# Kernel optimization log

Hardware: AMD Instinct MI355X
Metric: run time of the kernel (lower is better)

## Reference

```python
import jax, jax.numpy as jnp
import numpy as np

B, FH, FW, T = 128, 26, 26, 50
A, NUM_CLASSES = 5, 20
IGNORE_THRESH = 0.75
COORD_SCALE, NOOBJ_SCALE, OBJ_SCALE, CLASS_SCALE = 1.0, 1.0, 5.0, 1.0
ANCHORS = jnp.array([[1.3221, 1.73145], [3.19275, 4.00944], [5.05587, 8.09892],
                     [9.47112, 4.84053], [11.2364, 10.0071]], dtype=jnp.float32)


def xywh2xxyy(b):
    return jnp.stack([b[:, 0] - b[:, 2] / 2, b[:, 1] - b[:, 3] / 2,
                      b[:, 0] + b[:, 2] / 2, b[:, 1] + b[:, 3] / 2], axis=1)


def xxyy2xywh(b):
    return jnp.stack([(b[:, 0] + b[:, 2]) / 2, (b[:, 1] + b[:, 3]) / 2,
                      b[:, 2] - b[:, 0], b[:, 3] - b[:, 1]], axis=1)


def pair_iou(b1, b2):
    # b1: [N,4] xxyy, b2: [K,4] xxyy -> [N,K]
    xi1 = jnp.maximum(b1[:, None, 0], b2[None, :, 0])
    yi1 = jnp.maximum(b1[:, None, 1], b2[None, :, 1])
    xi2 = jnp.minimum(b1[:, None, 2], b2[None, :, 2])
    yi2 = jnp.minimum(b1[:, None, 3], b2[None, :, 3])
    inter = jnp.maximum(xi2 - xi1, 0.0) * jnp.maximum(yi2 - yi1, 0.0)
    a1 = ((b1[:, 2] - b1[:, 0]) * (b1[:, 3] - b1[:, 1]))[:, None]
    a2 = ((b2[:, 2] - b2[:, 0]) * (b2[:, 3] - b2[:, 1]))[None, :]
    return inter / (a1 + a2 - inter)


def make_all_anchors(F_H, F_W):
    ys, xs = jnp.meshgrid(jnp.arange(F_H), jnp.arange(F_W), indexing='ij')
    cells = jnp.stack([xs.ravel(), ys.ravel()], axis=-1).astype(jnp.float32)  # [K,2] (c_x, c_y)
    K = F_H * F_W
    all_anch = jnp.concatenate([jnp.broadcast_to(cells[:, None, :], (K, A, 2)),
                                jnp.broadcast_to(ANCHORS[None, :, :], (K, A, 2))], axis=-1)
    return all_anch.reshape(K * A, 4)  # (c_x, c_y, p_w, p_h), top-left-cell coords


def _build_target_single(box_deltas, gt, all_anch, anch_xxyy, F_H, F_W):
    # box_deltas: [K*A,4] (sig tx, sig ty, exp tw, exp th); gt: [T,5]
    K = F_H * F_W
    valid = gt[:, :4].sum(-1) > 0
    scale = jnp.array([F_W, F_H, F_W, F_H], dtype=jnp.float32)
    gt_xxyy = gt[:, :4] * scale  # [T,4] grid units
    # predicted boxes
    pred = jnp.stack([all_anch[:, 0] + box_deltas[:, 0], all_anch[:, 1] + box_deltas[:, 1],
                      all_anch[:, 2] * box_deltas[:, 2], all_anch[:, 3] * box_deltas[:, 3]], axis=1)
    pred_xxyy = xywh2xxyy(pred)
    ious = pair_iou(pred_xxyy, gt_xxyy)                       # [K*A, T]
    ious = jnp.where(valid[None, :], ious, -1.0)
    max_iou = ious.max(axis=-1)                               # [K*A]
    pos_any = jnp.any(max_iou > IGNORE_THRESH)
    iou_mask0 = jnp.where(pos_any & (max_iou >= IGNORE_THRESH), 0.0, NOOBJ_SCALE).reshape(K, A)
    # anchor-gt overlaps for responsibility assignment
    overlaps = pair_iou(anch_xxyy, gt_xxyy).reshape(K, A, T)
    gt_xcycwh = xxyy2xywh(gt_xxyy)                            # [T,4]
    cx = jnp.clip(jnp.floor(gt_xcycwh[:, 0]).astype(jnp.int32), 0, F_W - 1)
    cy = jnp.clip(jnp.floor(gt_xcycwh[:, 1]).astype(jnp.int32), 0, F_H - 1)
    cell = cy * F_W + cx                                      # [T]
    aidx = jnp.argmax(overlaps[cell, :, jnp.arange(T)], axis=-1)  # [T]
    anch_ka = all_anch.reshape(K, A, 4)
    assigned = anch_ka[cell, aidx]                            # [T,4]
    tgt_box = jnp.stack([gt_xcycwh[:, 0] - assigned[:, 0], gt_xcycwh[:, 1] - assigned[:, 1],
                         gt_xcycwh[:, 2] / assigned[:, 2], gt_xcycwh[:, 3] / assigned[:, 3]], axis=1)
    miou_t = max_iou.reshape(K, A)[cell, aidx]                # [T]
    cls_t = gt[:, 4]
    carry0 = (jnp.zeros((K, A)), iou_mask0, jnp.zeros((K, A, 4)),
              jnp.zeros((K, A)), jnp.zeros((K, A)), jnp.zeros((K, A)))
    def step(c, xs):
        it, im, bt, bm, ct, cm = c
        ce, an, v, tb, cl, mi = xs
        def w(arr, new):
            return arr.at[ce, an].set(jnp.where(v, new, arr[ce, an]))
        return (w(it, mi), w(im, OBJ_SCALE), w(bt, tb), w(bm, 1.0), w(ct, cl), w(cm, 1.0)), None
    (it, im, bt, bm, ct, cm), _ = jax.lax.scan(step, carry0, (cell, aidx, valid, tgt_box, cls_t, miou_t))
    return it, im, bt, bm, ct, cm


def setup_inputs() -> dict:
    key = jax.random.key(0)
    k1, k2, k3, k4, k5 = jax.random.split(key, 5)
    outputs = jax.random.normal(k1, (B, A * (5 + NUM_CLASSES), FH, FW), dtype=jnp.float32) * 0.1
    x1 = jax.random.uniform(k2, (B, T, 1), minval=0.02, maxval=0.75)
    y1 = jax.random.uniform(k3, (B, T, 1), minval=0.02, maxval=0.75)
    wh = jax.random.uniform(k4, (B, T, 2), minval=0.05, maxval=0.2)
    cls = jax.random.randint(k5, (B, T, 1), 0, NUM_CLASSES).astype(jnp.float32)
    targets = jnp.concatenate([x1, y1, x1 + wh[..., :1], y1 + wh[..., 1:]], axis=-1)
    targets = jnp.concatenate([targets, cls], axis=-1)  # [B, T, 5]
    return {"outputs": outputs, "targets": targets}


def reference(outputs, targets):
    Bn, _, F_H, F_W = outputs.shape
    out = outputs.transpose(0, 2, 3, 1).reshape(Bn, F_H * F_W * A, 5 + NUM_CLASSES)
    xy = jax.nn.sigmoid(out[..., 0:2])
    wh = jnp.exp(out[..., 2:4])
    conf = jax.nn.sigmoid(out[..., 4])            # [B, K*A]
    cls_score = out[..., 5:]                      # [B, K*A, C]
    box_delta = jnp.concatenate([xy, wh], axis=-1)  # [B, K*A, 4]
    all_anch = make_all_anchors(F_H, F_W)
    anch_xcycwh = all_anch.at[:, :2].add(0.5)
    anch_xxyy = xywh2xxyy(anch_xcycwh)
    it, im, bt, bm, ct, cm = jax.vmap(
        lambda d, g: _build_target_single(d, g, all_anch, anch_xxyy, F_H, F_W))(box_delta, targets)
    it = it.reshape(Bn, -1)
    im = im.reshape(Bn, -1)
    bt = bt.reshape(Bn, -1, 4)
    bm = bm.reshape(Bn, -1, 1)
    ct = ct.reshape(Bn, -1).astype(jnp.int32)
    cm = cm.reshape(Bn, -1)
    box_loss = COORD_SCALE * jnp.sum((box_delta * bm - bt * bm) ** 2) / 2.0 / Bn
    iou_loss = jnp.sum((conf * im - it * im) ** 2) / 2.0 / Bn
    logp = jax.nn.log_softmax(cls_score, axis=-1)
    ce = -jnp.take_along_axis(logp, ct[..., None], axis=-1)[..., 0]
    class_loss = CLASS_SCALE * jnp.sum(cm * ce) / Bn
    return box_loss + iou_loss + class_loss
```

## Files before the change

### kernel.cpp

```cpp
#include <hip/hip_runtime.h>
#include <math.h>

constexpr int BN = 128;
constexpr int FH = 26, FW = 26;
constexpr int T  = 50;
constexpr int A  = 5;
constexpr int NC = 20;
constexpr int K  = FH * FW;
constexpr int KA = K * A;
constexpr int CH = A * (5 + NC);
constexpr int REC = 12;

constexpr float IGNORE_THRESH = 0.75f;
constexpr float OBJ_SCALE = 5.0f;

constexpr int CHUNKS = (KA + 255) / 256;

__constant__ float ANCW[A] = {1.3221f, 3.19275f, 5.05587f, 9.47112f, 11.2364f};
__constant__ float ANCH[A] = {1.73145f, 4.00944f, 8.09892f, 4.84053f, 10.0071f};

__device__ __forceinline__ float sigmoidf(float x) {
    return 1.0f / (1.0f + expf(-x));
}

__global__ __launch_bounds__(256) void yolo_prep(
        const float* __restrict__ targets, float* __restrict__ gtrec,
        int* __restrict__ pos_any, float* __restrict__ s_masked,
        float* __restrict__ out) {
    int i = blockIdx.x * 256 + threadIdx.x;
    if (i == 0) out[0] = 0.0f;
    if (i < BN) { pos_any[i] = 0; s_masked[i] = 0.0f; }
    if (i >= BN * T) return;

    const float* g = targets + (size_t)i * 5;
    float rx1 = g[0], ry1 = g[1], rx2 = g[2], ry2 = g[3];
    bool valid = (rx1 + ry1 + rx2 + ry2) > 0.0f;
    float x1 = rx1 * FW, y1 = ry1 * FH, x2 = rx2 * FW, y2 = ry2 * FH;
    float w = x2 - x1, h = y2 - y1;

    float cxf = 0.5f * (x1 + x2), cyf = 0.5f * (y1 + y2);
    int cx = (int)floorf(cxf); cx = min(max(cx, 0), FW - 1);
    int cy = (int)floorf(cyf); cy = min(max(cy, 0), FH - 1);
    int cell = cy * FW + cx;

    float acx = (float)cx + 0.5f, acy = (float)cy + 0.5f;
    float best = -1.0f; int ai = 0;
    for (int a = 0; a < A; ++a) {
        float aw = ANCW[a], ah = ANCH[a];
        float xi1 = fmaxf(acx - 0.5f * aw, x1), yi1 = fmaxf(acy - 0.5f * ah, y1);
        float xi2 = fminf(acx + 0.5f * aw, x2), yi2 = fminf(acy + 0.5f * ah, y2);
        float inter = fmaxf(xi2 - xi1, 0.0f) * fmaxf(yi2 - yi1, 0.0f);
        float iou = inter / (aw * ah + w * h - inter);
        if (iou > best) { best = iou; ai = a; }
    }

    float* r = gtrec + (size_t)i * REC;
    r[0] = x1; r[1] = y1; r[2] = x2; r[3] = y2;
    r[4] = w * h;
    r[5] = valid ? 1.0f : 0.0f;
    r[6] = cxf - (float)cx;
    r[7] = cyf - (float)cy;
    r[8] = w / ANCW[ai];
    r[9] = h / ANCH[ai];
    r[10] = g[4];
    r[11] = valid ? (float)(ai * K + cell) : -1.0f;
}

__global__ __launch_bounds__(256) void yolo_main(
        const float* __restrict__ outputs, const float* __restrict__ gtrec,
        int* __restrict__ pos_any, float* __restrict__ s_masked,
        float* __restrict__ out) {
    __shared__ float ld[T * REC];
    __shared__ float redl[4], redm[4];
    __shared__ int   reda[4];

    const int b   = blockIdx.y;
    const int tid = threadIdx.x;
    for (int i = tid; i < T * REC; i += 256) ld[i] = gtrec[(size_t)b * T * REC + i];
    __syncthreads();

    const int s = blockIdx.x * 256 + tid;
    float loss = 0.0f, masked = 0.0f;
    int any = 0;

    if (s < KA) {
        const int a = s / K, k = s - a * K;
        const int y = k / FW, x = k - y * FW;
        const float* ob = outputs + (size_t)b * CH * K;

        float o0 = ob[(a * 25 + 0) * K + k];
        float o1 = ob[(a * 25 + 1) * K + k];
        float o2 = ob[(a * 25 + 2) * K + k];
        float o3 = ob[(a * 25 + 3) * K + k];
        float o4 = ob[(a * 25 + 4) * K + k];

        float s0 = sigmoidf(o0), s1 = sigmoidf(o1);
        float e2 = expf(o2),     e3 = expf(o3);
        float px = (float)x + s0, py = (float)y + s1;
        float pw = ANCW[a] * e2,  ph = ANCH[a] * e3;
        float px1 = px - 0.5f * pw, px2 = px + 0.5f * pw;
        float py1 = py - 0.5f * ph, py2 = py + 0.5f * ph;
        float parea = pw * ph;

        float m = -1.0f;
        int w = -1;
        for (int t = 0; t < T; ++t) {
            const float* r = &ld[t * REC];
            if (r[5] != 0.0f) {
                float xi1 = fmaxf(px1, r[0]), yi1 = fmaxf(py1, r[1]);
                float xi2 = fminf(px2, r[2]), yi2 = fminf(py2, r[3]);
                float inter = fmaxf(xi2 - xi1, 0.0f) * fmaxf(yi2 - yi1, 0.0f);
                float iou = inter / (parea + r[4] - inter);
                m = fmaxf(m, iou);
                if ((int)r[11] == s) w = t;
            }
        }
        any = (m > IGNORE_THRESH) ? 1 : 0;

        float conf = sigmoidf(o4);
        if (w >= 0) {
            float d = (conf - m) * OBJ_SCALE;
            loss += 0.5f * d * d;
            const float* r = &ld[w * REC];
            float d0 = s0 - r[6], d1 = s1 - r[7];
            float d2 = e2 - r[8], d3 = e3 - r[9];
            loss += 0.5f * (d0 * d0 + d1 * d1 + d2 * d2 + d3 * d3);

            float mx = -1e30f;
            for (int c = 0; c < NC; ++c)
                mx = fmaxf(mx, ob[(a * 25 + 5 + c) * K + k]);
            float se = 0.0f;
            for (int c = 0; c < NC; ++c)
                se += expf(ob[(a * 25 + 5 + c) * K + k] - mx);
            int cls = (int)r[10];
            loss += (logf(se) + mx) - ob[(a * 25 + 5 + cls) * K + k];
        } else {
            float term = 0.5f * conf * conf;
            loss += term;
            if (m >= IGNORE_THRESH) masked += term;
        }
    }

    for (int off = 32; off > 0; off >>= 1) {
        loss   += __shfl_down(loss, off);
        masked += __shfl_down(masked, off);
    }
    any = __any(any) ? 1 : 0;
    int lane = tid & 63, wv = tid >> 6;
    if (lane == 0) { redl[wv] = loss; redm[wv] = masked; reda[wv] = any; }
    __syncthreads();
    if (tid == 0) {
        float L = redl[0] + redl[1] + redl[2] + redl[3];
        float M = redm[0] + redm[1] + redm[2] + redm[3];
        int   An = reda[0] | reda[1] | reda[2] | reda[3];
        atomicAdd(out, L * (1.0f / (float)BN));
        if (M != 0.0f) atomicAdd(&s_masked[b], M);
        if (An) atomicOr(&pos_any[b], 1);
    }
}

__global__ __launch_bounds__(128) void yolo_fix(
        const int* __restrict__ pos_any, const float* __restrict__ s_masked,
        float* __restrict__ out) {
    __shared__ float red[2];
    int tid = threadIdx.x;
    float v = (tid < BN && pos_any[tid]) ? s_masked[tid] : 0.0f;
    for (int off = 32; off > 0; off >>= 1) v += __shfl_down(v, off);
    if ((tid & 63) == 0) red[tid >> 6] = v;
    __syncthreads();
    if (tid == 0) atomicAdd(out, -(red[0] + red[1]) * (1.0f / (float)BN));
}

extern "C" void kernel_launch(void* const* d_in, const int* in_sizes, int n_in,
                              void* d_out, int out_size, void* d_ws, size_t ws_size,
                              hipStream_t stream) {
    const float* outputs = (const float*)d_in[0];
    const float* targets = (const float*)d_in[1];
    float* out = (float*)d_out;

    float* gtrec    = (float*)d_ws;
    int*   pos_any  = (int*)((char*)d_ws + (size_t)BN * T * REC * 4);
    float* s_masked = (float*)((char*)pos_any + BN * sizeof(int));

    yolo_prep<<<(BN * T + 255) / 256, 256, 0, stream>>>(targets, gtrec, pos_any, s_masked, out);
    yolo_main<<<dim3(CHUNKS, BN), 256, 0, stream>>>(outputs, gtrec, pos_any, s_masked, out);
    yolo_fix<<<1, 128, 0, stream>>>(pos_any, s_masked, out);
}
```

Measured before the change: 110.6 us.

## Fuse target prep into main kernel, drop atomics, use fast math intrinsics

Removes the separate prep kernel by having each block compute its own per-image ground-truth records in shared memory, which saves one launch and a global round trip. Cross-block atomics are replaced by per-block partial sums that the final kernel reduces deterministically. Invalid boxes are encoded as empty boxes so the IoU loop has no branch, and the loop and class loads are unrolled. Sigmoid, exp, log and division now use fast hardware intrinsics, which costs some accuracy, and the prep work is recomputed in each of the blocks per image.

```diff
diff --git a/kernel.cpp b/kernel.cpp
--- a/kernel.cpp
+++ b/kernel.cpp
@@ -9,74 +9,68 @@
 constexpr int K  = FH * FW;
 constexpr int KA = K * A;
 constexpr int CH = A * (5 + NC);
-constexpr int REC = 12;
 
 constexpr float IGNORE_THRESH = 0.75f;
 constexpr float OBJ_SCALE = 5.0f;
 
 constexpr int CHUNKS = (KA + 255) / 256;
+constexpr int NPART  = BN * CHUNKS;
 
 __constant__ float ANCW[A] = {1.3221f, 3.19275f, 5.05587f, 9.47112f, 11.2364f};
 __constant__ float ANCH[A] = {1.73145f, 4.00944f, 8.09892f, 4.84053f, 10.0071f};
 
-__device__ __forceinline__ float sigmoidf(float x) {
-    return 1.0f / (1.0f + expf(-x));
-}
-
-__global__ __launch_bounds__(256) void yolo_prep(
-        const float* __restrict__ targets, float* __restrict__ gtrec,
-        int* __restrict__ pos_any, float* __restrict__ s_masked,
-        float* __restrict__ out) {
-    int i = blockIdx.x * 256 + threadIdx.x;
-    if (i == 0) out[0] = 0.0f;
-    if (i < BN) { pos_any[i] = 0; s_masked[i] = 0.0f; }
-    if (i >= BN * T) return;
-
-    const float* g = targets + (size_t)i * 5;
-    float rx1 = g[0], ry1 = g[1], rx2 = g[2], ry2 = g[3];
-    bool valid = (rx1 + ry1 + rx2 + ry2) > 0.0f;
-    float x1 = rx1 * FW, y1 = ry1 * FH, x2 = rx2 * FW, y2 = ry2 * FH;
-    float w = x2 - x1, h = y2 - y1;
-
-    float cxf = 0.5f * (x1 + x2), cyf = 0.5f * (y1 + y2);
-    int cx = (int)floorf(cxf); cx = min(max(cx, 0), FW - 1);
-    int cy = (int)floorf(cyf); cy = min(max(cy, 0), FH - 1);
-    int cell = cy * FW + cx;
-
-    float acx = (float)cx + 0.5f, acy = (float)cy + 0.5f;
-    float best = -1.0f; int ai = 0;
-    for (int a = 0; a < A; ++a) {
-        float aw = ANCW[a], ah = ANCH[a];
-        float xi1 = fmaxf(acx - 0.5f * aw, x1), yi1 = fmaxf(acy - 0.5f * ah, y1);
-        float xi2 = fminf(acx + 0.5f * aw, x2), yi2 = fminf(acy + 0.5f * ah, y2);
-        float inter = fmaxf(xi2 - xi1, 0.0f) * fmaxf(yi2 - yi1, 0.0f);
-        float iou = inter / (aw * ah + w * h - inter);
-        if (iou > best) { best = iou; ai = a; }
-    }
-
-    float* r = gtrec + (size_t)i * REC;
-    r[0] = x1; r[1] = y1; r[2] = x2; r[3] = y2;
-    r[4] = w * h;
-    r[5] = valid ? 1.0f : 0.0f;
-    r[6] = cxf - (float)cx;
-    r[7] = cyf - (float)cy;
-    r[8] = w / ANCW[ai];
-    r[9] = h / ANCH[ai];
-    r[10] = g[4];
-    r[11] = valid ? (float)(ai * K + cell) : -1.0f;
+__device__ __forceinline__ float fast_sigmoid(float x) {
+    return __builtin_amdgcn_rcpf(1.0f + __expf(-x));
 }
 
 __global__ __launch_bounds__(256) void yolo_main(
-        const float* __restrict__ outputs, const float* __restrict__ gtrec,
-        int* __restrict__ pos_any, float* __restrict__ s_masked,
-        float* __restrict__ out) {
-    __shared__ float ld[T * REC];
-    __shared__ float redl[4], redm[4];
-    __shared__ int   reda[4];
+        const float* __restrict__ outputs,
+        const float* __restrict__ targets,
+        float* __restrict__ Lp, float* __restrict__ Mp, int* __restrict__ Anyp) {
+    __shared__ float4 sbox[T];
+    __shared__ float2 sas[T];
+    __shared__ float4 stb[T];
+    __shared__ float  scls[T];
+    __shared__ float  redl[4], redm[4];
+    __shared__ int    reda[4];
 
     const int b   = blockIdx.y;
     const int tid = threadIdx.x;
-    for (int i = tid; i < T * REC; i += 256) ld[i] = gtrec[(size_t)b * T * REC + i];
+
+    if (tid < T) {
+        const float* g = targets + ((size_t)b * T + tid) * 5;
+        float rx1 = g[0], ry1 = g[1], rx2 = g[2], ry2 = g[3];
+        bool valid = (rx1 + ry1 + rx2 + ry2) > 0.0f;
+        float x1 = rx1 * FW, y1 = ry1 * FH, x2 = rx2 * FW, y2 = ry2 * FH;
+        float w = x2 - x1, h = y2 - y1;
+
+        float cxf = 0.5f * (x1 + x2), cyf = 0.5f * (y1 + y2);
+        int cx = (int)floorf(cxf); cx = min(max(cx, 0), FW - 1);
+        int cy = (int)floorf(cyf); cy = min(max(cy, 0), FH - 1);
+        int cell = cy * FW + cx;
+
+        float acx = (float)cx + 0.5f, acy = (float)cy + 0.5f;
+        float best = -1.0f; int ai = 0;
+        for (int a = 0; a < A; ++a) {
+            float aw = ANCW[a], ah = ANCH[a];
+            float xi1 = fmaxf(acx - 0.5f * aw, x1), yi1 = fmaxf(acy - 0.5f * ah, y1);
+            float xi2 = fminf(acx + 0.5f * aw, x2), yi2 = fminf(acy + 0.5f * ah, y2);
+            float inter = fmaxf(xi2 - xi1, 0.0f) * fmaxf(yi2 - yi1, 0.0f);
+            float iou = inter / (aw * ah + w * h - inter);
+            if (iou > best) { best = iou; ai = a; }
+        }
+
+        if (valid) {
+            sbox[tid] = make_float4(x1, y1, x2, y2);
+            sas[tid]  = make_float2(w * h, __int_as_float(ai * K + cell));
+        } else {
+            sbox[tid] = make_float4(1e18f, 1e18f, -1e18f, -1e18f);
+            sas[tid]  = make_float2(1.0f, __int_as_float(-1));
+        }
+        stb[tid]  = make_float4(cxf - (float)cx, cyf - (float)cy,
+                                w / ANCW[ai], h / ANCH[ai]);
+        scls[tid] = g[4];
+    }
     __syncthreads();
 
     const int s = blockIdx.x * 256 + tid;
@@ -94,8 +88,8 @@
         float o3 = ob[(a * 25 + 3) * K + k];
         float o4 = ob[(a * 25 + 4) * K + k];
 
-        float s0 = sigmoidf(o0), s1 = sigmoidf(o1);
-        float e2 = expf(o2),     e3 = expf(o3);
+        float s0 = fast_sigmoid(o0), s1 = fast_sigmoid(o1);
+        float e2 = __expf(o2),       e3 = __expf(o3);
         float px = (float)x + s0, py = (float)y + s1;
         float pw = ANCW[a] * e2,  ph = ANCH[a] * e3;
         float px1 = px - 0.5f * pw, px2 = px + 0.5f * pw;
@@ -104,36 +98,40 @@
 
         float m = -1.0f;
         int w = -1;
+        #pragma unroll 10
         for (int t = 0; t < T; ++t) {
-            const float* r = &ld[t * REC];
-            if (r[5] != 0.0f) {
-                float xi1 = fmaxf(px1, r[0]), yi1 = fmaxf(py1, r[1]);
-                float xi2 = fminf(px2, r[2]), yi2 = fminf(py2, r[3]);
-                float inter = fmaxf(xi2 - xi1, 0.0f) * fmaxf(yi2 - yi1, 0.0f);
-                float iou = inter / (parea + r[4] - inter);
-                m = fmaxf(m, iou);
-                if ((int)r[11] == s) w = t;
-            }
+            float4 bx  = sbox[t];
+            float2 as2 = sas[t];
+            float xi1 = fmaxf(px1, bx.x), yi1 = fmaxf(py1, bx.y);
+            float xi2 = fminf(px2, bx.z), yi2 = fminf(py2, bx.w);
+            float iw = fmaxf(xi2 - xi1, 0.0f), ih = fmaxf(yi2 - yi1, 0.0f);
+            float inter = iw * ih;
+            float iou = inter * __builtin_amdgcn_rcpf(parea + as2.x - inter);
+            m = fmaxf(m, iou);
+            if (__float_as_int(as2.y) == s) w = t;
         }
         any = (m > IGNORE_THRESH) ? 1 : 0;
 
-        float conf = sigmoidf(o4);
+        float conf = fast_sigmoid(o4);
         if (w >= 0) {
             float d = (conf - m) * OBJ_SCALE;
             loss += 0.5f * d * d;
-            const float* r = &ld[w * REC];
-            float d0 = s0 - r[6], d1 = s1 - r[7];
-            float d2 = e2 - r[8], d3 = e3 - r[9];
+            float4 tb = stb[w];
+            float d0 = s0 - tb.x, d1 = s1 - tb.y;
+            float d2 = e2 - tb.z, d3 = e3 - tb.w;
             loss += 0.5f * (d0 * d0 + d1 * d1 + d2 * d2 + d3 * d3);
 
-            float mx = -1e30f;
-            for (int c = 0; c < NC; ++c)
-                mx = fmaxf(mx, ob[(a * 25 + 5 + c) * K + k]);
+            float v[NC];
+            #pragma unroll
+            for (int c = 0; c < NC; ++c) v[c] = ob[(a * 25 + 5 + c) * K + k];
+            float mx = v[0];
+            #pragma unroll
+            for (int c = 1; c < NC; ++c) mx = fmaxf(mx, v[c]);
             float se = 0.0f;
-            for (int c = 0; c < NC; ++c)
-                se += expf(ob[(a * 25 + 5 + c) * K + k] - mx);
-            int cls = (int)r[10];
-            loss += (logf(se) + mx) - ob[(a * 25 + 5 + cls) * K + k];
+            #pragma unroll
+            for (int c = 0; c < NC; ++c) se += __expf(v[c] - mx);
+            int cls = (int)scls[w];
+            loss += (__logf(se) + mx) - v[cls];
         } else {
             float term = 0.5f * conf * conf;
             loss += term;
@@ -150,25 +148,34 @@
     if (lane == 0) { redl[wv] = loss; redm[wv] = masked; reda[wv] = any; }
     __syncthreads();
     if (tid == 0) {
-        float L = redl[0] + redl[1] + redl[2] + redl[3];
-        float M = redm[0] + redm[1] + redm[2] + redm[3];
-        int   An = reda[0] | reda[1] | reda[2] | reda[3];
-        atomicAdd(out, L * (1.0f / (float)BN));
-        if (M != 0.0f) atomicAdd(&s_masked[b], M);
-        if (An) atomicOr(&pos_any[b], 1);
+        int idx = b * CHUNKS + blockIdx.x;
+        Lp[idx]   = redl[0] + redl[1] + redl[2] + redl[3];
+        Mp[idx]   = redm[0] + redm[1] + redm[2] + redm[3];
+        Anyp[idx] = reda[0] | reda[1] | reda[2] | reda[3];
     }
 }
 
 __global__ __launch_bounds__(128) void yolo_fix(
-        const int* __restrict__ pos_any, const float* __restrict__ s_masked,
-        float* __restrict__ out) {
+        const float* __restrict__ Lp, const float* __restrict__ Mp,
+        const int* __restrict__ Anyp, float* __restrict__ out) {
     __shared__ float red[2];
     int tid = threadIdx.x;
-    float v = (tid < BN && pos_any[tid]) ? s_masked[tid] : 0.0f;
-    for (int off = 32; off > 0; off >>= 1) v += __shfl_down(v, off);
-    if ((tid & 63) == 0) red[tid >> 6] = v;
+    float L = 0.0f, M = 0.0f;
+    int any = 0;
+    if (tid < BN) {
+        #pragma unroll
+        for (int c = 0; c < CHUNKS; ++c) {
+            int idx = tid * CHUNKS + c;
+            L += Lp[idx];
+            M += Mp[idx];
+            any |= Anyp[idx];
+        }
+    }
+    float acc = L - (any ? M : 0.0f);
+    for (int off = 32; off > 0; off >>= 1) acc += __shfl_down(acc, off);
+    if ((tid & 63) == 0) red[tid >> 6] = acc;
     __syncthreads();
-    if (tid == 0) atomicAdd(out, -(red[0] + red[1]) * (1.0f / (float)BN));
+    if (tid == 0) out[0] = (red[0] + red[1]) * (1.0f / (float)BN);
 }
 
 extern "C" void kernel_launch(void* const* d_in, const int* in_sizes, int n_in,
@@ -178,11 +185,10 @@
     const float* targets = (const float*)d_in[1];
     float* out = (float*)d_out;
 
-    float* gtrec    = (float*)d_ws;
-    int*   pos_any  = (int*)((char*)d_ws + (size_t)BN * T * REC * 4);
-    float* s_masked = (float*)((char*)pos_any + BN * sizeof(int));
+    float* Lp   = (float*)d_ws;
+    float* Mp   = Lp + NPART;
+    int*   Anyp = (int*)(Mp + NPART);
 
-    yolo_prep<<<(BN * T + 255) / 256, 256, 0, stream>>>(targets, gtrec, pos_any, s_masked, out);
-    yolo_main<<<dim3(CHUNKS, BN), 256, 0, stream>>>(outputs, gtrec, pos_any, s_masked, out);
-    yolo_fix<<<1, 128, 0, stream>>>(pos_any, s_masked, out);
+    yolo_main<<<dim3(CHUNKS, BN), 256, 0, stream>>>(outputs, targets, Lp, Mp, Anyp);
+    yolo_fix<<<1, 128, 0, stream>>>(Lp, Mp, Anyp, out);
 }
```

Result: faster. 93.00 us (-15.9%).
